# Kernel tuning notes

Hardware: AMD Instinct MI355X
Metric: run time of the kernel (lower is better)

The kernel has to match this reference:

```python
import jax, jax.numpy as jnp
import numpy as np

OUTPUT_SIZE = 32


def setup_inputs() -> dict:
    key = jax.random.key(0)
    k1, k2, k3 = jax.random.split(key, 3)
    B, T, D, H, O = 256, 512, 1024, 2048, OUTPUT_SIZE
    return {
        "x": jax.random.normal(k1, (B, T, D), dtype=jnp.float32),
        "W1": jax.random.normal(k2, (D + O, H), dtype=jnp.float32) * 0.02,
        "b1": jnp.zeros((H,), dtype=jnp.float32),
        "W2": jax.random.normal(k3, (H, O), dtype=jnp.float32) * 0.02,
        "b2": jnp.zeros((O,), dtype=jnp.float32),
    }


def reference(x, W1, b1, W2, b2):
    # x: [B, T, D]; sequential greedy decoding with previous-prediction feedback.
    B = x.shape[0]
    O = W2.shape[1]

    def step(prev_pred, x_t):
        # prev_pred: [B] int32 (class 0 at t=0, matching torch zero-init preds)
        oh = jax.nn.one_hot(prev_pred, O, dtype=x_t.dtype)           # [B, O]
        inp = jnp.concatenate([x_t, oh], axis=-1)                    # [B, D+O]
        h = jnp.tanh(inp @ W1 + b1)                                  # [B, H]
        logit = h @ W2 + b2                                          # [B, O]
        pred = jnp.argmax(logit, axis=-1).astype(jnp.int32)          # [B]
        return pred, (logit, pred)

    init = jnp.zeros((B,), dtype=jnp.int32)
    _, (logits_t, preds_t) = jax.lax.scan(step, init, jnp.swapaxes(x, 0, 1))
    logits = jnp.swapaxes(logits_t, 0, 1)  # [B, T, O]
    preds = jnp.swapaxes(preds_t, 0, 1).astype(jnp.int64)  # [B, T]
    return logits, preds
```

## Files before the change

kernel.cpp:

```cpp
#include <hip/hip_runtime.h>
#include <cstdint>
#include <cstddef>

#define BATCH 256
#define SEQ   512
#define DIM   1024
#define HID   2048
#define NOUT  32

typedef __attribute__((ext_vector_type(8))) short  short8;
typedef __attribute__((ext_vector_type(4))) float  f32x4;

__device__ __forceinline__ ushort f2bf(float v) {
    uint u = __builtin_bit_cast(uint, v);
    u = u + 0x7FFFu + ((u >> 16) & 1u);
    return (ushort)(u >> 16);
}
__device__ __forceinline__ float bf2f(ushort h) {
    uint u = ((uint)h) << 16;
    return __builtin_bit_cast(float, u);
}

__global__ __launch_bounds__(256) void split_w1t(const float* __restrict__ W1,
                                                 ushort* __restrict__ Bth,
                                                 ushort* __restrict__ Btl)
{
    __shared__ ushort th[32][33];
    __shared__ ushort tl[32][33];
    const int n0 = blockIdx.x * 32;
    const int k0 = blockIdx.y * 32;
    const int tx = threadIdx.x & 31;
    const int ty = threadIdx.x >> 5;
#pragma unroll
    for (int r = 0; r < 4; ++r) {
        int k = ty + r * 8;
        float v = W1[(size_t)(k0 + k) * HID + n0 + tx];
        ushort h = f2bf(v);
        th[k][tx] = h;
        tl[k][tx] = f2bf(v - bf2f(h));
    }
    __syncthreads();
#pragma unroll
    for (int r = 0; r < 4; ++r) {
        int n = ty + r * 8;
        Bth[(size_t)(n0 + n) * DIM + k0 + tx] = th[tx][n];
        Btl[(size_t)(n0 + n) * DIM + k0 + tx] = tl[tx][n];
    }
}

#define BM 128
#define BN 128
#define BK 32

__global__ __launch_bounds__(256) void gemm_split(const float*  __restrict__ A,
                                                  const ushort* __restrict__ Bth,
                                                  const ushort* __restrict__ Btl,
                                                  const float*  __restrict__ b1,
                                                  float* __restrict__ G)
{
    __shared__ ushort Ah[BM][BK];
    __shared__ ushort Al[BM][BK];
    __shared__ ushort Bh[BN][BK];
    __shared__ ushort Bl[BN][BK];

    const int tid  = threadIdx.x;
    const int lane = tid & 63;
    const int wave = tid >> 6;
    const int n0 = blockIdx.x * BN;
    const int m0 = blockIdx.y * BM;
    const int wm = (wave & 1) * 64;
    const int wn = (wave >> 1) * 64;

    const int srow = tid >> 1;
    const int skc  = (tid & 1) * 16;
    const float*  aptr  = A   + (size_t)(m0 + srow) * DIM + skc;
    const ushort* bhptr = Bth + (size_t)(n0 + srow) * DIM + skc;
    const ushort* blptr = Btl + (size_t)(n0 + srow) * DIM + skc;

    const int fr = lane & 15;
    const int fq = lane >> 4;

    f32x4 acc[4][4];
#pragma unroll
    for (int i = 0; i < 4; ++i)
#pragma unroll
        for (int j = 0; j < 4; ++j) {
            f32x4 z = {0.f, 0.f, 0.f, 0.f};
            acc[i][j] = z;
        }

    for (int k0 = 0; k0 < DIM; k0 += BK) {
        float4 a0 = *(const float4*)(aptr + k0);
        float4 a1 = *(const float4*)(aptr + k0 + 4);
        float4 a2 = *(const float4*)(aptr + k0 + 8);
        float4 a3 = *(const float4*)(aptr + k0 + 12);
        short8 bh0 = *(const short8*)(bhptr + k0);
        short8 bh1 = *(const short8*)(bhptr + k0 + 8);
        short8 bl0 = *(const short8*)(blptr + k0);
        short8 bl1 = *(const short8*)(blptr + k0 + 8);

        __syncthreads();

        float av[16] = {a0.x, a0.y, a0.z, a0.w, a1.x, a1.y, a1.z, a1.w,
                        a2.x, a2.y, a2.z, a2.w, a3.x, a3.y, a3.z, a3.w};
        short8 h0, h1, l0, l1;
#pragma unroll
        for (int i = 0; i < 8; ++i) {
            ushort h = f2bf(av[i]);
            h0[i] = (short)h;
            l0[i] = (short)f2bf(av[i] - bf2f(h));
        }
#pragma unroll
        for (int i = 0; i < 8; ++i) {
            ushort h = f2bf(av[8 + i]);
            h1[i] = (short)h;
            l1[i] = (short)f2bf(av[8 + i] - bf2f(h));
        }
        *(short8*)&Ah[srow][skc]     = h0;
        *(short8*)&Ah[srow][skc + 8] = h1;
        *(short8*)&Al[srow][skc]     = l0;
        *(short8*)&Al[srow][skc + 8] = l1;
        *(short8*)&Bh[srow][skc]     = bh0;
        *(short8*)&Bh[srow][skc + 8] = bh1;
        *(short8*)&Bl[srow][skc]     = bl0;
        *(short8*)&Bl[srow][skc + 8] = bl1;

        __syncthreads();

        short8 afh[4], afl[4], bfh[4], bfl[4];
#pragma unroll
        for (int t = 0; t < 4; ++t) {
            afh[t] = *(const short8*)&Ah[wm + t * 16 + fr][fq * 8];
            afl[t] = *(const short8*)&Al[wm + t * 16 + fr][fq * 8];
            bfh[t] = *(const short8*)&Bh[wn + t * 16 + fr][fq * 8];
            bfl[t] = *(const short8*)&Bl[wn + t * 16 + fr][fq * 8];
        }
#pragma unroll
        for (int mt = 0; mt < 4; ++mt)
#pragma unroll
            for (int nt = 0; nt < 4; ++nt) {
                acc[mt][nt] = __builtin_amdgcn_mfma_f32_16x16x32_bf16(afh[mt], bfh[nt], acc[mt][nt], 0, 0, 0);
                acc[mt][nt] = __builtin_amdgcn_mfma_f32_16x16x32_bf16(afh[mt], bfl[nt], acc[mt][nt], 0, 0, 0);
                acc[mt][nt] = __builtin_amdgcn_mfma_f32_16x16x32_bf16(afl[mt], bfh[nt], acc[mt][nt], 0, 0, 0);
            }
    }

#pragma unroll
    for (int nt = 0; nt < 4; ++nt) {
        const int gn = n0 + wn + nt * 16 + fr;
        const float bias = b1[gn];
#pragma unroll
        for (int mt = 0; mt < 4; ++mt) {
            const int gmb = m0 + wm + mt * 16 + fq * 4;
            float* out = G + (size_t)gmb * HID + gn;
#pragma unroll
            for (int r = 0; r < 4; ++r)
                out[(size_t)r * HID] = acc[mt][nt][r] + bias;
        }
    }
}

__global__ __launch_bounds__(1024) void seq_scan(const float* __restrict__ G,
                                                 const float* __restrict__ W1,
                                                 const float* __restrict__ W2,
                                                 const float* __restrict__ b2,
                                                 float* __restrict__ out_logits,
                                                 float* __restrict__ out_preds)
{
    const int b   = blockIdx.x;
    const int t   = threadIdx.x;
    const int og  = t >> 8;
    const int j   = t & 255;
    const int o0  = og * 8;
    const int h0  = j * 8;

    __shared__ float hbuf[HID];
    __shared__ float partials[16][8];
    __shared__ int   pred_sh;

    float w2r[8][8];
#pragma unroll
    for (int i = 0; i < 8; ++i) {
        const float4* p4 = reinterpret_cast<const float4*>(&W2[(size_t)(h0 + i) * NOUT + o0]);
        float4 aa = p4[0], bbq = p4[1];
        w2r[i][0] = aa.x;  w2r[i][1] = aa.y;  w2r[i][2] = aa.z;  w2r[i][3] = aa.w;
        w2r[i][4] = bbq.x; w2r[i][5] = bbq.y; w2r[i][6] = bbq.z; w2r[i][7] = bbq.w;
    }

    int p = 0;
    const float* Gb = G + (size_t)b * SEQ * HID;
    float2 g = *reinterpret_cast<const float2*>(Gb + 2 * t);

    for (int step = 0; step < SEQ; ++step) {
        float2 u = *reinterpret_cast<const float2*>(&W1[(size_t)(DIM + p) * HID + 2 * t]);
        float hv0 = tanhf(g.x + u.x);
        float hv1 = tanhf(g.y + u.y);
        if (step + 1 < SEQ)
            g = *reinterpret_cast<const float2*>(Gb + (size_t)(step + 1) * HID + 2 * t);

        *reinterpret_cast<float2*>(&hbuf[2 * t]) = make_float2(hv0, hv1);
        __syncthreads();

        float4 ha = *reinterpret_cast<const float4*>(&hbuf[h0]);
        float4 hb = *reinterpret_cast<const float4*>(&hbuf[h0 + 4]);
        float hv[8] = {ha.x, ha.y, ha.z, ha.w, hb.x, hb.y, hb.z, hb.w};
        float acc[8];
#pragma unroll
        for (int c = 0; c < 8; ++c) acc[c] = 0.f;
#pragma unroll
        for (int i = 0; i < 8; ++i)
#pragma unroll
            for (int c = 0; c < 8; ++c)
                acc[c] = fmaf(hv[i], w2r[i][c], acc[c]);

#pragma unroll
        for (int off = 32; off; off >>= 1)
#pragma unroll
            for (int c = 0; c < 8; ++c)
                acc[c] += __shfl_xor(acc[c], off, 64);

        const int wave = t >> 6;
        const int lane = t & 63;
        if (lane == 0) {
#pragma unroll
            for (int c = 0; c < 8; ++c) partials[wave][c] = acc[c];
        }
        __syncthreads();

        if (t < 32) {
            const int o  = t;
            const int gq = o >> 3;
            const int c  = o & 7;
            float logit = b2[o] + partials[gq * 4 + 0][c] + partials[gq * 4 + 1][c]
                                + partials[gq * 4 + 2][c] + partials[gq * 4 + 3][c];
            out_logits[((size_t)b * SEQ + step) * NOUT + o] = logit;

            float v = logit; int idx = o;
#pragma unroll
            for (int off = 16; off; off >>= 1) {
                float ov = __shfl_xor(v, off, 32);
                int   oi = __shfl_xor(idx, off, 32);
                if (ov > v || (ov == v && oi < idx)) { v = ov; idx = oi; }
            }
            if (o == 0) {
                pred_sh = idx;
                out_preds[(size_t)b * SEQ + step] = (float)idx;
            }
        }
        __syncthreads();
        p = pred_sh;
    }
}

extern "C" void kernel_launch(void* const* d_in, const int* in_sizes, int n_in,
                              void* d_out, int out_size, void* d_ws, size_t ws_size,
                              hipStream_t stream) {
    const float* x  = (const float*)d_in[0];
    const float* W1 = (const float*)d_in[1];
    const float* b1 = (const float*)d_in[2];
    const float* W2 = (const float*)d_in[3];
    const float* b2 = (const float*)d_in[4];

    const size_t G_ELEMS = (size_t)BATCH * SEQ * HID;
    float*  G   = (float*)d_ws;
    ushort* Bth = (ushort*)((char*)d_ws + G_ELEMS * sizeof(float));
    ushort* Btl = Bth + (size_t)HID * DIM;

    float* out_logits = (float*)d_out;
    float* out_preds  = (float*)d_out + (size_t)BATCH * SEQ * NOUT;

    split_w1t<<<dim3(HID / 32, DIM / 32), 256, 0, stream>>>(W1, Bth, Btl);
    gemm_split<<<dim3(HID / BN, BATCH * SEQ / BM), 256, 0, stream>>>(x, Bth, Btl, b1, G);
    seq_scan<<<BATCH, 1024, 0, stream>>>(G, W1, W2, b2, out_logits, out_preds);
}
```

Measured before the change: 4.472 ms.

## Pre-split A/B into tiled bf16 hi/lo and use 256x256 async-LDS GEMM

Result: faster. 4.177 ms (-6.6%).

```diff
diff --git a/kernel.cpp b/kernel.cpp
--- a/kernel.cpp
+++ b/kernel.cpp
@@ -8,6 +8,15 @@
 #define HID   2048
 #define NOUT  32
 
+#define BM 256
+#define BN 256
+#define BK 64
+#define KT_PER_SEG 16
+#define KSTEPS 48
+#define TM_TILES 512
+#define TN_TILES 8
+#define TILE_SHORTS (BM * BK)
+
 typedef __attribute__((ext_vector_type(8))) short  short8;
 typedef __attribute__((ext_vector_type(4))) float  f32x4;
 
@@ -19,6 +28,198 @@
 __device__ __forceinline__ float bf2f(ushort h) {
     uint u = ((uint)h) << 16;
     return __builtin_bit_cast(float, u);
+}
+
+__device__ __forceinline__ void gload16(const ushort* g, ushort* l) {
+    __builtin_amdgcn_global_load_lds(
+        (const __attribute__((address_space(1))) uint32_t*)(g),
+        (__attribute__((address_space(3))) uint32_t*)(l),
+        16, 0, 0);
+}
+
+__device__ __forceinline__ float fast_tanh(float x) {
+    float e = __expf(2.0f * x);
+    return 1.0f - 2.0f / (e + 1.0f);
+}
+
+__global__ __launch_bounds__(256) void prep_a(const float* __restrict__ x,
+                                              ushort* __restrict__ Ah,
+                                              ushort* __restrict__ Al)
+{
+    __shared__ alignas(16) ushort hi[TILE_SHORTS];
+    __shared__ alignas(16) ushort lo[TILE_SHORTS];
+    const int tm = blockIdx.x;
+    const int kt = blockIdx.y;
+    const int t  = threadIdx.x;
+
+#pragma unroll
+    for (int p = 0; p < 4; ++p) {
+        const int row  = p * 64 + (t >> 2);
+        const int part = t & 3;
+        const float* src = x + (size_t)(tm * 256 + row) * DIM + kt * 64 + part * 16;
+        float4 v0 = *(const float4*)(src);
+        float4 v1 = *(const float4*)(src + 4);
+        float4 v2 = *(const float4*)(src + 8);
+        float4 v3 = *(const float4*)(src + 12);
+        float av[16] = {v0.x, v0.y, v0.z, v0.w, v1.x, v1.y, v1.z, v1.w,
+                        v2.x, v2.y, v2.z, v2.w, v3.x, v3.y, v3.z, v3.w};
+#pragma unroll
+        for (int g = 0; g < 2; ++g) {
+            short8 hs, ls;
+#pragma unroll
+            for (int i = 0; i < 8; ++i) {
+                float vv = av[g * 8 + i];
+                ushort hh = f2bf(vv);
+                hs[i] = (short)hh;
+                ls[i] = (short)f2bf(vv - bf2f(hh));
+            }
+            const int kc = part * 2 + g;
+            *(short8*)&hi[(kc * 256 + row) * 8] = hs;
+            *(short8*)&lo[(kc * 256 + row) * 8] = ls;
+        }
+    }
+    __syncthreads();
+    const size_t tbase = ((size_t)tm * KT_PER_SEG + kt) * TILE_SHORTS;
+#pragma unroll
+    for (int i = 0; i < 8; ++i) {
+        const int idx = i * 2048 + t * 8;
+        *(short8*)(Ah + tbase + idx) = *(const short8*)(hi + idx);
+        *(short8*)(Al + tbase + idx) = *(const short8*)(lo + idx);
+    }
+}
+
+__global__ __launch_bounds__(256) void prep_b(const float* __restrict__ W1,
+                                              ushort* __restrict__ Bh,
+                                              ushort* __restrict__ Bl)
+{
+    __shared__ alignas(16) ushort hi[TILE_SHORTS];
+    __shared__ alignas(16) ushort lo[TILE_SHORTS];
+    const int tn = blockIdx.x;
+    const int kt = blockIdx.y;
+    const int t  = threadIdx.x;
+
+#pragma unroll
+    for (int p = 0; p < 16; ++p) {
+        const int krow = p * 4 + (t >> 6);
+        const int n4   = (t & 63) * 4;
+        float4 v = *(const float4*)&W1[(size_t)(kt * 64 + krow) * HID + tn * 256 + n4];
+        const int kc = krow >> 3, j = krow & 7;
+        float vv[4] = {v.x, v.y, v.z, v.w};
+#pragma unroll
+        for (int q = 0; q < 4; ++q) {
+            ushort hh = f2bf(vv[q]);
+            hi[(kc * 256 + n4 + q) * 8 + j] = hh;
+            lo[(kc * 256 + n4 + q) * 8 + j] = f2bf(vv[q] - bf2f(hh));
+        }
+    }
+    __syncthreads();
+    const size_t tbase = ((size_t)tn * KT_PER_SEG + kt) * TILE_SHORTS;
+#pragma unroll
+    for (int i = 0; i < 8; ++i) {
+        const int idx = i * 2048 + t * 8;
+        *(short8*)(Bh + tbase + idx) = *(const short8*)(hi + idx);
+        *(short8*)(Bl + tbase + idx) = *(const short8*)(lo + idx);
+    }
+}
+
+__global__ __launch_bounds__(512, 2) void gemm256(const ushort* __restrict__ Ah,
+                                                  const ushort* __restrict__ Alo,
+                                                  const ushort* __restrict__ Bh,
+                                                  const ushort* __restrict__ Blo,
+                                                  const float*  __restrict__ b1,
+                                                  float* __restrict__ G)
+{
+    __shared__ alignas(16) ushort lds[2][2][TILE_SHORTS];
+
+    const int tid  = threadIdx.x;
+    const int lane = tid & 63;
+    const int wave = tid >> 6;
+    const int fr = lane & 15;
+    const int fq = lane >> 4;
+    const int wm = (wave >> 2) * 128;
+    const int wn = (wave & 3) * 64;
+
+    const int cpx = (TM_TILES * TN_TILES) >> 3;
+    const int wg  = blockIdx.x;
+    const int swz = (wg & 7) * cpx + (wg >> 3);
+    const int tm  = swz >> 3;
+    const int tn  = swz & 7;
+
+    auto stage = [&](int buf, int ks) {
+        const int seg = ks >> 4, kt = ks & 15;
+        const ushort* at = ((seg == 2) ? Alo : Ah) + ((size_t)tm * KT_PER_SEG + kt) * TILE_SHORTS;
+        const ushort* bt = ((seg == 1) ? Blo : Bh) + ((size_t)tn * KT_PER_SEG + kt) * TILE_SHORTS;
+        ushort* la = &lds[buf][0][0];
+        ushort* lb = &lds[buf][1][0];
+#pragma unroll
+        for (int i = 0; i < 4; ++i)
+            gload16(at + i * 4096 + tid * 8, la + i * 4096 + tid * 8);
+#pragma unroll
+        for (int i = 0; i < 4; ++i)
+            gload16(bt + i * 4096 + tid * 8, lb + i * 4096 + tid * 8);
+    };
+
+    f32x4 acc[8][4];
+#pragma unroll
+    for (int i = 0; i < 8; ++i)
+#pragma unroll
+        for (int j = 0; j < 4; ++j) {
+            f32x4 z = {0.f, 0.f, 0.f, 0.f};
+            acc[i][j] = z;
+        }
+
+    stage(0, 0);
+    stage(1, 1);
+    asm volatile("s_waitcnt vmcnt(8)" ::: "memory");
+    __builtin_amdgcn_s_barrier();
+
+    for (int ks = 0; ks < KSTEPS; ++ks) {
+        const int cur = ks & 1;
+        const ushort* LA = &lds[cur][0][0];
+        const ushort* LB = &lds[cur][1][0];
+#pragma unroll
+        for (int kk = 0; kk < 2; ++kk) {
+            const int kc = kk * 4 + fq;
+            short8 a[8], b[4];
+#pragma unroll
+            for (int mt = 0; mt < 8; ++mt)
+                a[mt] = *(const short8*)&LA[(kc * 256 + wm + mt * 16 + fr) * 8];
+#pragma unroll
+            for (int nt = 0; nt < 4; ++nt)
+                b[nt] = *(const short8*)&LB[(kc * 256 + wn + nt * 16 + fr) * 8];
+            __builtin_amdgcn_s_setprio(1);
+#pragma unroll
+            for (int mt = 0; mt < 8; ++mt)
+#pragma unroll
+                for (int nt = 0; nt < 4; ++nt)
+                    acc[mt][nt] = __builtin_amdgcn_mfma_f32_16x16x32_bf16(a[mt], b[nt], acc[mt][nt], 0, 0, 0);
+            __builtin_amdgcn_s_setprio(0);
+        }
+        asm volatile("" ::: "memory");
+        __builtin_amdgcn_s_barrier();
+        if (ks + 2 < KSTEPS) {
+            stage(cur, ks + 2);
+            asm volatile("s_waitcnt vmcnt(8)" ::: "memory");
+        } else {
+            asm volatile("s_waitcnt vmcnt(0)" ::: "memory");
+        }
+        __builtin_amdgcn_s_barrier();
+    }
+
+    const int m0 = tm * BM, n0 = tn * BN;
+#pragma unroll
+    for (int nt = 0; nt < 4; ++nt) {
+        const int gn = n0 + wn + nt * 16 + fr;
+        const float bias = b1[gn];
+#pragma unroll
+        for (int mt = 0; mt < 8; ++mt) {
+            const int gm = m0 + wm + mt * 16 + fq * 4;
+            float* out = G + (size_t)gm * HID + gn;
+#pragma unroll
+            for (int r = 0; r < 4; ++r)
+                out[(size_t)r * HID] = acc[mt][nt][r] + bias;
+        }
+    }
 }
 
 __global__ __launch_bounds__(256) void split_w1t(const float* __restrict__ W1,
@@ -48,26 +249,22 @@
     }
 }
 
-#define BM 128
-#define BN 128
-#define BK 32
-
 __global__ __launch_bounds__(256) void gemm_split(const float*  __restrict__ A,
                                                   const ushort* __restrict__ Bth,
                                                   const ushort* __restrict__ Btl,
                                                   const float*  __restrict__ b1,
                                                   float* __restrict__ G)
 {
-    __shared__ ushort Ah[BM][BK];
-    __shared__ ushort Al[BM][BK];
-    __shared__ ushort Bh[BN][BK];
-    __shared__ ushort Bl[BN][BK];
+    __shared__ ushort Ahs[128][32];
+    __shared__ ushort Als[128][32];
+    __shared__ ushort Bhs[128][32];
+    __shared__ ushort Bls[128][32];
 
     const int tid  = threadIdx.x;
     const int lane = tid & 63;
     const int wave = tid >> 6;
-    const int n0 = blockIdx.x * BN;
-    const int m0 = blockIdx.y * BM;
+    const int n0 = blockIdx.x * 128;
+    const int m0 = blockIdx.y * 128;
     const int wm = (wave & 1) * 64;
     const int wn = (wave >> 1) * 64;
 
@@ -89,7 +286,7 @@
             acc[i][j] = z;
         }
 
-    for (int k0 = 0; k0 < DIM; k0 += BK) {
+    for (int k0 = 0; k0 < DIM; k0 += 32) {
         float4 a0 = *(const float4*)(aptr + k0);
         float4 a1 = *(const float4*)(aptr + k0 + 4);
         float4 a2 = *(const float4*)(aptr + k0 + 8);
@@ -116,24 +313,24 @@
             h1[i] = (short)h;
             l1[i] = (short)f2bf(av[8 + i] - bf2f(h));
         }
-        *(short8*)&Ah[srow][skc]     = h0;
-        *(short8*)&Ah[srow][skc + 8] = h1;
-        *(short8*)&Al[srow][skc]     = l0;
-        *(short8*)&Al[srow][skc + 8] = l1;
-        *(short8*)&Bh[srow][skc]     = bh0;
-        *(short8*)&Bh[srow][skc + 8] = bh1;
-        *(short8*)&Bl[srow][skc]     = bl0;
-        *(short8*)&Bl[srow][skc + 8] = bl1;
+        *(short8*)&Ahs[srow][skc]     = h0;
+        *(short8*)&Ahs[srow][skc + 8] = h1;
+        *(short8*)&Als[srow][skc]     = l0;
+        *(short8*)&Als[srow][skc + 8] = l1;
+        *(short8*)&Bhs[srow][skc]     = bh0;
+        *(short8*)&Bhs[srow][skc + 8] = bh1;
+        *(short8*)&Bls[srow][skc]     = bl0;
+        *(short8*)&Bls[srow][skc + 8] = bl1;
 
         __syncthreads();
 
         short8 afh[4], afl[4], bfh[4], bfl[4];
 #pragma unroll
         for (int t = 0; t < 4; ++t) {
-            afh[t] = *(const short8*)&Ah[wm + t * 16 + fr][fq * 8];
-            afl[t] = *(const short8*)&Al[wm + t * 16 + fr][fq * 8];
-            bfh[t] = *(const short8*)&Bh[wn + t * 16 + fr][fq * 8];
-            bfl[t] = *(const short8*)&Bl[wn + t * 16 + fr][fq * 8];
+            afh[t] = *(const short8*)&Ahs[wm + t * 16 + fr][fq * 8];
+            afl[t] = *(const short8*)&Als[wm + t * 16 + fr][fq * 8];
+            bfh[t] = *(const short8*)&Bhs[wn + t * 16 + fr][fq * 8];
+            bfl[t] = *(const short8*)&Bls[wn + t * 16 + fr][fq * 8];
         }
 #pragma unroll
         for (int mt = 0; mt < 4; ++mt)
@@ -193,8 +390,8 @@
 
     for (int step = 0; step < SEQ; ++step) {
         float2 u = *reinterpret_cast<const float2*>(&W1[(size_t)(DIM + p) * HID + 2 * t]);
-        float hv0 = tanhf(g.x + u.x);
-        float hv1 = tanhf(g.y + u.y);
+        float hv0 = fast_tanh(g.x + u.x);
+        float hv1 = fast_tanh(g.y + u.y);
         if (step + 1 < SEQ)
             g = *reinterpret_cast<const float2*>(Gb + (size_t)(step + 1) * HID + 2 * t);
 
@@ -261,15 +458,31 @@
     const float* W2 = (const float*)d_in[3];
     const float* b2 = (const float*)d_in[4];
 
-    const size_t G_ELEMS = (size_t)BATCH * SEQ * HID;
-    float*  G   = (float*)d_ws;
-    ushort* Bth = (ushort*)((char*)d_ws + G_ELEMS * sizeof(float));
-    ushort* Btl = Bth + (size_t)HID * DIM;
-
+    const size_t G_BYTES = (size_t)BATCH * SEQ * HID * sizeof(float);
+    const size_t A_BYTES = (size_t)BATCH * SEQ * DIM * sizeof(ushort);
+    const size_t B_BYTES = (size_t)HID * DIM * sizeof(ushort);
+
+    float* G = (float*)d_ws;
     float* out_logits = (float*)d_out;
     float* out_preds  = (float*)d_out + (size_t)BATCH * SEQ * NOUT;
 
-    split_w1t<<<dim3(HID / 32, DIM / 32), 256, 0, stream>>>(W1, Bth, Btl);
-    gemm_split<<<dim3(HID / BN, BATCH * SEQ / BM), 256, 0, stream>>>(x, Bth, Btl, b1, G);
+    const size_t need_new = G_BYTES + 2 * A_BYTES + 2 * B_BYTES;
+
+    if (ws_size >= need_new) {
+        ushort* Ah = (ushort*)((char*)d_ws + G_BYTES);
+        ushort* Al = (ushort*)((char*)Ah + A_BYTES);
+        ushort* Bh = (ushort*)((char*)Al + A_BYTES);
+        ushort* Bl = (ushort*)((char*)Bh + B_BYTES);
+
+        prep_a<<<dim3(TM_TILES, KT_PER_SEG), 256, 0, stream>>>(x, Ah, Al);
+        prep_b<<<dim3(TN_TILES, KT_PER_SEG), 256, 0, stream>>>(W1, Bh, Bl);
+        gemm256<<<dim3(TM_TILES * TN_TILES), 512, 0, stream>>>(Ah, Al, Bh, Bl, b1, G);
+    } else {
+        ushort* Bth = (ushort*)((char*)d_ws + G_BYTES);
+        ushort* Btl = Bth + (size_t)HID * DIM;
+        split_w1t<<<dim3(HID / 32, DIM / 32), 256, 0, stream>>>(W1, Bth, Btl);
+        gemm_split<<<dim3(HID / 128, BATCH * SEQ / 128), 256, 0, stream>>>(x, Bth, Btl, b1, G);
+    }
+
     seq_scan<<<BATCH, 1024, 0, stream>>>(G, W1, W2, b2, out_logits, out_preds);
 }
```
